# Performance work log

Measured on AMD Instinct MI355X. Metric: run time of the kernel, lower is better.

The kernel has to match this reference:

```python
import jax, jax.numpy as jnp
import numpy as np

D_MODEL = 1024
NHEAD = 16
HEAD_DIM = D_MODEL // NHEAD
DFF = 4096
EPS = 1e-5


def _layer_norm(x, gamma, beta):
    mu = jnp.mean(x, axis=-1, keepdims=True)
    var = jnp.mean(jnp.square(x - mu), axis=-1, keepdims=True)
    return (x - mu) * jax.lax.rsqrt(var + EPS) * gamma + beta


def setup_inputs() -> dict:
    key = jax.random.key(0)
    ks = jax.random.split(key, 16)
    s = 1.0 / np.sqrt(D_MODEL)
    sf = 1.0 / np.sqrt(DFF)
    inp = {
        "x": jax.random.normal(ks[0], (4, 4096, D_MODEL), dtype=jnp.float32),
        "wq": jax.random.uniform(ks[1], (D_MODEL, D_MODEL), jnp.float32, -s, s),
        "bq": jnp.zeros((D_MODEL,), jnp.float32),
        "wk": jax.random.uniform(ks[2], (D_MODEL, D_MODEL), jnp.float32, -s, s),
        "bk": jnp.zeros((D_MODEL,), jnp.float32),
        "wv": jax.random.uniform(ks[3], (D_MODEL, D_MODEL), jnp.float32, -s, s),
        "bv": jnp.zeros((D_MODEL,), jnp.float32),
        "wo": jax.random.uniform(ks[4], (D_MODEL, D_MODEL), jnp.float32, -s, s),
        "bo": jnp.zeros((D_MODEL,), jnp.float32),
        "w1": jax.random.uniform(ks[5], (D_MODEL, 2 * DFF), jnp.float32, -s, s),
        "b1": jnp.zeros((2 * DFF,), jnp.float32),
        "w2": jax.random.uniform(ks[6], (DFF, D_MODEL), jnp.float32, -sf, sf),
        "b2": jnp.zeros((D_MODEL,), jnp.float32),
        "g1": jnp.ones((D_MODEL,), jnp.float32),
        "be1": jnp.zeros((D_MODEL,), jnp.float32),
        "g2": jnp.ones((D_MODEL,), jnp.float32),
        "be2": jnp.zeros((D_MODEL,), jnp.float32),
    }
    return inp


def reference(x, wq, bq, wk, bk, wv, bv, wo, bo, w1, b1, w2, b2, g1, be1, g2, be2):
    B, S, _ = x.shape
    # --- sublayer 1: pre-norm + linear attention ---
    h = _layer_norm(x, g1, be1)
    q = (h @ wq + bq).reshape(B, S, NHEAD, HEAD_DIM).transpose(0, 2, 1, 3)
    k = (h @ wk + bk).reshape(B, S, NHEAD, HEAD_DIM).transpose(0, 2, 1, 3)
    v = (h @ wv + bv).reshape(B, S, NHEAD, HEAD_DIM).transpose(0, 2, 1, 3)
    q = jax.nn.elu(q) + 1.0
    k = jax.nn.elu(k) + 1.0
    # kv: [B,H,d,e] = sum_s k[...,s,d] v[...,s,e]  (O(n) linear attention)
    kv = jnp.einsum("bhsd,bhse->bhde", k, v)
    attn = jnp.einsum("bhsd,bhde->bhse", q, kv)
    attn = attn.transpose(0, 2, 1, 3).reshape(B, S, D_MODEL)
    x = x + (attn @ wo + bo)
    # --- sublayer 2: pre-norm + GEGLU FFN ---
    h = _layer_norm(x, g2, be2)
    ff = h @ w1 + b1
    g, lin = ff[..., :DFF], ff[..., DFF:]
    ff = jax.nn.gelu(g, approximate=False) * lin
    x = x + (ff @ w2 + b2)
    return x
```

## Files before the change

kernel.cpp:

```cpp
#include <hip/hip_runtime.h>

typedef unsigned short u16;
typedef u16  u16x2  __attribute__((ext_vector_type(2)));
typedef u16  u16x4  __attribute__((ext_vector_type(4)));
typedef u16  u16x8  __attribute__((ext_vector_type(8)));
typedef float f32x4 __attribute__((ext_vector_type(4)));
typedef __bf16 bf16x8 __attribute__((ext_vector_type(8)));

#define D_MODEL 1024
#define DFF     4096
#define SEQ     4096
#define BATCH   4
#define NHEAD   16
#define MROWS   (BATCH*SEQ)
#define MCHUNK  4096

#define BM 128
#define BN 128
#define BK 32

__device__ __forceinline__ float bf2f(u16 u) {
  unsigned v = ((unsigned)u) << 16;
  return __builtin_bit_cast(float, v);
}
__device__ __forceinline__ u16 f2bf(float f) {
  unsigned u = __builtin_bit_cast(unsigned, f);
  u += 0x7fffu + ((u >> 16) & 1u);
  return (u16)(u >> 16);
}

__device__ __forceinline__ void gload16(void* lds, const void* g) {
  __builtin_amdgcn_global_load_lds(
      (const __attribute__((address_space(1))) unsigned*)g,
      (__attribute__((address_space(3))) unsigned*)lds, 16, 0, 0);
}

__device__ __forceinline__ void barrier_raw() {
  asm volatile("" ::: "memory");
  __builtin_amdgcn_s_barrier();
  asm volatile("" ::: "memory");
}
#define VMWAIT(n) asm volatile("s_waitcnt vmcnt(" #n ")" ::: "memory")

__device__ __forceinline__ int xcd_swz_bid() {
  const int gx = gridDim.x;
  const int nwg = gx * gridDim.y;
  int bid = blockIdx.y * gx + blockIdx.x;
  const int cpx = nwg >> 3;
  return (bid & 7) * cpx + (bid >> 3);
}

__global__ __launch_bounds__(256)
void transpose_kernel(const float* __restrict__ W, u16* __restrict__ Wt, int K, int N)
{
  __shared__ u16 tile[32][33];
  const int n0 = blockIdx.x * 32, k0 = blockIdx.y * 32;
  const int tx = threadIdx.x & 31, ty = threadIdx.x >> 5;
#pragma unroll
  for (int r = ty; r < 32; r += 8)
    tile[r][tx] = f2bf(W[(size_t)(k0 + r) * N + n0 + tx]);
  __syncthreads();
#pragma unroll
  for (int r = ty; r < 32; r += 8)
    Wt[(size_t)(n0 + r) * K + k0 + tx] = tile[tx][r];
}

template<typename T>
__global__ __launch_bounds__(256)
void ln_kernel(const T* __restrict__ x, const float* __restrict__ g,
               const float* __restrict__ be, u16* __restrict__ out)
{
  const int row = blockIdx.x;
  const int t = threadIdx.x;
  float v0, v1, v2, v3;
  if constexpr (sizeof(T) == 4) {
    f32x4 u = ((const f32x4*)((const float*)x + (size_t)row * D_MODEL))[t];
    v0 = u.x; v1 = u.y; v2 = u.z; v3 = u.w;
  } else {
    u16x4 u = ((const u16x4*)((const u16*)x + (size_t)row * D_MODEL))[t];
    v0 = bf2f(u.x); v1 = bf2f(u.y); v2 = bf2f(u.z); v3 = bf2f(u.w);
  }
  float s  = v0 + v1 + v2 + v3;
  float s2 = v0*v0 + v1*v1 + v2*v2 + v3*v3;
#pragma unroll
  for (int off = 32; off > 0; off >>= 1) {
    s  += __shfl_down(s,  off);
    s2 += __shfl_down(s2, off);
  }
  __shared__ float red[8];
  if ((t & 63) == 0) { red[t >> 6] = s; red[4 + (t >> 6)] = s2; }
  __syncthreads();
  float S  = red[0] + red[1] + red[2] + red[3];
  float S2 = red[4] + red[5] + red[6] + red[7];
  float mu  = S * (1.f / D_MODEL);
  float var = S2 * (1.f / D_MODEL) - mu * mu;
  var = fmaxf(var, 0.f);
  float rs  = rsqrtf(var + 1e-5f);
  f32x4 gu = ((const f32x4*)g)[t];
  f32x4 bu = ((const f32x4*)be)[t];
  u16x4 o;
  o.x = f2bf((v0 - mu) * rs * gu.x + bu.x);
  o.y = f2bf((v1 - mu) * rs * gu.y + bu.y);
  o.z = f2bf((v2 - mu) * rs * gu.z + bu.z);
  o.w = f2bf((v3 - mu) * rs * gu.w + bu.w);
  ((u16x4*)(out + (size_t)row * D_MODEL))[t] = o;
}

template<int MODE>
__global__ __launch_bounds__(256, 2)
void gemm_kernel(const u16* __restrict__ A, const u16* __restrict__ Bt,
                 const float* __restrict__ bias, const void* __restrict__ resv,
                 void* __restrict__ outv, int N, int K)
{
  __shared__ __align__(16) u16 lA[3][BM * BK];
  __shared__ __align__(16) u16 lB[3][BN * BK];
  const float* resf = (const float*)resv;
  const u16*   resb = (const u16*)resv;
  const int tid = threadIdx.x;
  const int wave = tid >> 6, lane = tid & 63;
  const int quad = lane >> 4, ln = lane & 15;
  const int bid = xcd_swz_bid();
  const int bm = (bid / (int)gridDim.x) * BM, bn = (bid % (int)gridDim.x) * BN;
  const int wm = (wave >> 1) * 64, wn = (wave & 1) * 64;

  f32x4 acc[4][4] = {};

  const int c0 = tid,       r0 = c0 >> 2, q0 = c0 & 3;
  const int c1 = tid + 256, r1 = c1 >> 2, q1 = c1 & 3;
  const u16* gA0 = A  + (size_t)(bm + r0) * K + q0 * 8;
  const u16* gA1 = A  + (size_t)(bm + r1) * K + q1 * 8;
  const u16* gB0 = Bt + (size_t)(bn + r0) * K + q0 * 8;
  const u16* gB1 = Bt + (size_t)(bn + r1) * K + q1 * 8;
  const int d0 = wave * 64 * 8;
  const int d1 = (256 + wave * 64) * 8;

  const int nk = K / BK;
  gload16(&lA[0][d0], gA0);
  gload16(&lA[0][d1], gA1);
  gload16(&lB[0][d0], gB0);
  gload16(&lB[0][d1], gB1);
  gload16(&lA[1][d0], gA0 + BK);
  gload16(&lA[1][d1], gA1 + BK);
  gload16(&lB[1][d0], gB0 + BK);
  gload16(&lB[1][d1], gB1 + BK);

  int cur = 0;
  for (int t = 0; t < nk; ++t) {
    if (t + 2 < nk) {
      int wb = cur + 2; if (wb >= 3) wb -= 3;
      const size_t ko = (size_t)(t + 2) * BK;
      gload16(&lA[wb][d0], gA0 + ko);
      gload16(&lA[wb][d1], gA1 + ko);
      gload16(&lB[wb][d0], gB0 + ko);
      gload16(&lB[wb][d1], gB1 + ko);
      VMWAIT(8);
    } else if (t + 1 < nk) {
      VMWAIT(4);
    } else {
      VMWAIT(0);
    }
    barrier_raw();
    bf16x8 af[4], bfr[4];
#pragma unroll
    for (int i = 0; i < 4; ++i) {
      af[i]  = *(const bf16x8*)&lA[cur][(wm + i * 16 + ln) * BK + quad * 8];
      bfr[i] = *(const bf16x8*)&lB[cur][(wn + i * 16 + ln) * BK + quad * 8];
    }
#pragma unroll
    for (int i = 0; i < 4; ++i)
#pragma unroll
      for (int j = 0; j < 4; ++j)
        acc[i][j] = __builtin_amdgcn_mfma_f32_16x16x32_bf16(af[i], bfr[j], acc[i][j], 0, 0, 0);
    barrier_raw();
    cur = cur + 1; if (cur >= 3) cur = 0;
  }

#pragma unroll
  for (int j = 0; j < 4; ++j) {
    const int col = bn + wn + j * 16 + ln;
    const float bv = bias[col];
#pragma unroll
    for (int i = 0; i < 4; ++i) {
#pragma unroll
      for (int r = 0; r < 4; ++r) {
        const int row = bm + wm + i * 16 + quad * 4 + r;
        const size_t off = (size_t)row * N + col;
        float vv = acc[i][j][r] + bv;
        if (MODE == 1) vv = vv > 0.f ? vv + 1.f : __expf(vv);
        if (MODE == 2) vv += resf[off];
        if (MODE == 3) vv += bf2f(resb[off]);
        if (MODE == 3) ((float*)outv)[off] = vv;
        else           ((u16*)outv)[off]   = f2bf(vv);
      }
    }
  }
}

__global__ __launch_bounds__(256, 2)
void ffn1_kernel(const u16* __restrict__ A, const u16* __restrict__ Wt,
                 const float* __restrict__ b1, u16* __restrict__ out, int K)
{
  __shared__ __align__(16) u16 lA [2][BM * BK];
  __shared__ __align__(16) u16 lBg[2][BN * BK];
  __shared__ __align__(16) u16 lBl[2][BN * BK];
  const int tid = threadIdx.x;
  const int wave = tid >> 6, lane = tid & 63;
  const int quad = lane >> 4, ln = lane & 15;
  const int bm = blockIdx.y * BM, bn = blockIdx.x * BN;
  const int wm = (wave >> 1) * 64, wn = (wave & 1) * 64;

  f32x4 accg[4][4] = {};
  f32x4 accl[4][4] = {};

  const int c0 = tid,       r0 = c0 >> 2, q0 = c0 & 3;
  const int c1 = tid + 256, r1 = c1 >> 2, q1 = c1 & 3;
  const u16* gA0 = A  + (size_t)(bm + r0) * K + q0 * 8;
  const u16* gA1 = A  + (size_t)(bm + r1) * K + q1 * 8;
  const u16* gG0 = Wt + (size_t)(bn + r0) * K + q0 * 8;
  const u16* gG1 = Wt + (size_t)(bn + r1) * K + q1 * 8;
  const u16* gL0 = Wt + (size_t)(DFF + bn + r0) * K + q0 * 8;
  const u16* gL1 = Wt + (size_t)(DFF + bn + r1) * K + q1 * 8;
  const int d0 = wave * 64 * 8;
  const int d1 = (256 + wave * 64) * 8;

  const int nk = K / BK;
  gload16(&lA [0][d0], gA0);
  gload16(&lA [0][d1], gA1);
  gload16(&lBg[0][d0], gG0);
  gload16(&lBg[0][d1], gG1);
  gload16(&lBl[0][d0], gL0);
  gload16(&lBl[0][d1], gL1);

  int cur = 0;
  for (int t = 0; t < nk; ++t) {
    if (t + 1 < nk) {
      const int nxt = cur ^ 1;
      const size_t ko = (size_t)(t + 1) * BK;
      gload16(&lA [nxt][d0], gA0 + ko);
      gload16(&lA [nxt][d1], gA1 + ko);
      gload16(&lBg[nxt][d0], gG0 + ko);
      gload16(&lBg[nxt][d1], gG1 + ko);
      gload16(&lBl[nxt][d0], gL0 + ko);
      gload16(&lBl[nxt][d1], gL1 + ko);
      VMWAIT(6);
    } else {
      VMWAIT(0);
    }
    barrier_raw();
    bf16x8 af[4], bg[4], bl[4];
#pragma unroll
    for (int i = 0; i < 4; ++i) {
      af[i] = *(const bf16x8*)&lA [cur][(wm + i * 16 + ln) * BK + quad * 8];
      bg[i] = *(const bf16x8*)&lBg[cur][(wn + i * 16 + ln) * BK + quad * 8];
      bl[i] = *(const bf16x8*)&lBl[cur][(wn + i * 16 + ln) * BK + quad * 8];
    }
#pragma unroll
    for (int i = 0; i < 4; ++i)
#pragma unroll
      for (int j = 0; j < 4; ++j) {
        accg[i][j] = __builtin_amdgcn_mfma_f32_16x16x32_bf16(af[i], bg[j], accg[i][j], 0, 0, 0);
        accl[i][j] = __builtin_amdgcn_mfma_f32_16x16x32_bf16(af[i], bl[j], accl[i][j], 0, 0, 0);
      }
    barrier_raw();
    cur ^= 1;
  }

#pragma unroll
  for (int j = 0; j < 4; ++j) {
    const int col = bn + wn + j * 16 + ln;
    const float bgv = b1[col];
    const float blv = b1[DFF + col];
#pragma unroll
    for (int i = 0; i < 4; ++i) {
#pragma unroll
      for (int r = 0; r < 4; ++r) {
        const int row = bm + wm + i * 16 + quad * 4 + r;
        float gg = accg[i][j][r] + bgv;
        float ll = accl[i][j][r] + blv;
        float ge = 0.5f * gg * (1.f + erff(gg * 0.70710678118f));
        out[(size_t)row * DFF + col] = f2bf(ge * ll);
      }
    }
  }
}

#define KVCH 1024
__global__ __launch_bounds__(256)
void kvmm_kernel(const u16* __restrict__ kk, const u16* __restrict__ vv,
                 float* __restrict__ kvpart)
{
  __shared__ __align__(16) u16 lK[32][66];
  __shared__ __align__(16) u16 lV[32][66];
  const int blk = blockIdx.x;
  const int c = blk & 3, bh = blk >> 2;
  const int b = bh >> 4, h = bh & 15;
  const int tid = threadIdx.x, wave = tid >> 6, lane = tid & 63;
  const int quad = lane >> 4, ln = lane & 15;
  const int dbase = (wave >> 1) * 32, ebase = (wave & 1) * 32;
  f32x4 acc[2][2] = {};

  const int srow = tid >> 3;
  const int dcol = (tid & 7) * 8;
  const size_t gbase = ((size_t)b * SEQ + (size_t)c * KVCH + srow) * D_MODEL + h * 64 + dcol;
  const u16* gk = kk + gbase;
  const u16* gv = vv + gbase;

  for (int s0 = 0; s0 < KVCH; s0 += 32) {
    u16x8 k8 = *(const u16x8*)(gk + (size_t)s0 * D_MODEL);
    u16x8 v8 = *(const u16x8*)(gv + (size_t)s0 * D_MODEL);
    __syncthreads();
    u16x2* wk2 = (u16x2*)&lK[srow][dcol];
    u16x2* wv2 = (u16x2*)&lV[srow][dcol];
#pragma unroll
    for (int p = 0; p < 4; ++p) {
      u16x2 a; a.x = k8[2*p]; a.y = k8[2*p+1]; wk2[p] = a;
      u16x2 w; w.x = v8[2*p]; w.y = v8[2*p+1]; wv2[p] = w;
    }
    __syncthreads();
    bf16x8 af[2], bf[2];
#pragma unroll
    for (int i = 0; i < 2; ++i) {
      const int dd = dbase + i * 16 + ln;
      const int ee = ebase + i * 16 + ln;
      u16x8 at, bt;
#pragma unroll
      for (int j = 0; j < 8; ++j) {
        at[j] = lK[quad * 8 + j][dd];
        bt[j] = lV[quad * 8 + j][ee];
      }
      af[i] = __builtin_bit_cast(bf16x8, at);
      bf[i] = __builtin_bit_cast(bf16x8, bt);
    }
#pragma unroll
    for (int i = 0; i < 2; ++i)
#pragma unroll
      for (int j = 0; j < 2; ++j)
        acc[i][j] = __builtin_amdgcn_mfma_f32_16x16x32_bf16(af[i], bf[j], acc[i][j], 0, 0, 0);
  }

  float* op = kvpart + ((size_t)c * 64 + bh) * 4096;
#pragma unroll
  for (int i = 0; i < 2; ++i)
#pragma unroll
    for (int j = 0; j < 2; ++j)
#pragma unroll
      for (int r = 0; r < 4; ++r) {
        const int d = dbase + i * 16 + quad * 4 + r;
        const int e = ebase + j * 16 + ln;
        op[d * 64 + e] = acc[i][j][r];
      }
}

__global__ __launch_bounds__(256)
void kvreduce_kernel(float* __restrict__ p)
{
  const int i = blockIdx.x * 256 + threadIdx.x;
  f32x4* p4 = (f32x4*)p;
  f32x4 a = p4[i];
  f32x4 b = p4[i + 65536];
  f32x4 c = p4[i + 131072];
  f32x4 d = p4[i + 196608];
  p4[i] = (a + b) + (c + d);
}

__global__ __launch_bounds__(256)
void attn_kernel(const u16* __restrict__ qq, const float* __restrict__ kv,
                 u16* __restrict__ out)
{
  __shared__ __align__(16) float kvs[64 * 64];
  const int blk = blockIdx.x;
  const int sc = blk & 63;
  const int bh = blk >> 6;
  const int b = bh >> 4, h = bh & 15;
  const int t = threadIdx.x;
  const f32x4* src = (const f32x4*)(kv + (size_t)bh * 4096);
  for (int i = t; i < 1024; i += 256) ((f32x4*)kvs)[i] = src[i];
  __syncthreads();
  const int sl = t >> 2, e0 = (t & 3) * 16;
  const size_t row = (size_t)b * SEQ + sc * 64 + sl;
  const u16* qp = qq + row * D_MODEL + h * 64;
  float qv[64];
#pragma unroll
  for (int i = 0; i < 16; ++i) {
    u16x4 u = ((const u16x4*)qp)[i];
    qv[i*4+0] = bf2f(u.x); qv[i*4+1] = bf2f(u.y);
    qv[i*4+2] = bf2f(u.z); qv[i*4+3] = bf2f(u.w);
  }
  f32x4 acc[4] = {};
  for (int d = 0; d < 64; ++d) {
    const float qd = qv[d];
    const f32x4* kr = (const f32x4*)(kvs + d * 64 + e0);
#pragma unroll
    for (int i = 0; i < 4; ++i) acc[i] += qd * kr[i];
  }
  u16* op = out + row * D_MODEL + h * 64 + e0;
#pragma unroll
  for (int i = 0; i < 4; ++i) {
    u16x4 o;
    o.x = f2bf(acc[i][0]); o.y = f2bf(acc[i][1]);
    o.z = f2bf(acc[i][2]); o.w = f2bf(acc[i][3]);
    ((u16x4*)op)[i] = o;
  }
}

extern "C" void kernel_launch(void* const* d_in, const int* in_sizes, int n_in,
                              void* d_out, int out_size, void* d_ws, size_t ws_size,
                              hipStream_t stream)
{
  const float* x   = (const float*)d_in[0];
  const float* wq  = (const float*)d_in[1];
  const float* bq  = (const float*)d_in[2];
  const float* wk  = (const float*)d_in[3];
  const float* bk  = (const float*)d_in[4];
  const float* wv  = (const float*)d_in[5];
  const float* bv  = (const float*)d_in[6];
  const float* wo  = (const float*)d_in[7];
  const float* bo  = (const float*)d_in[8];
  const float* w1  = (const float*)d_in[9];
  const float* b1  = (const float*)d_in[10];
  const float* w2  = (const float*)d_in[11];
  const float* b2  = (const float*)d_in[12];
  const float* g1  = (const float*)d_in[13];
  const float* be1 = (const float*)d_in[14];
  const float* g2  = (const float*)d_in[15];
  const float* be2 = (const float*)d_in[16];

  char* ws = (char*)d_ws;
  const size_t MB = 1024ull * 1024ull;
  u16* wqt = (u16*)(ws + 0 * MB);
  u16* wkt = (u16*)(ws + 2 * MB);
  u16* wvt = (u16*)(ws + 4 * MB);
  u16* wot = (u16*)(ws + 6 * MB);
  u16* w1t = (u16*)(ws + 8 * MB);
  u16* w2t = (u16*)(ws + 24 * MB);

  u16* hb    = (u16*)(ws + 32 * MB);
  u16* x1b   = (u16*)(ws + 32 * MB);
  u16* kb    = (u16*)(ws + 64 * MB);
  u16* qb    = (u16*)(ws + 64 * MB);
  u16* hb2   = (u16*)(ws + 64 * MB);
  u16* vb    = (u16*)(ws + 96 * MB);
  u16* attnb = (u16*)(ws + 96 * MB);
  u16* gbuf  = (u16*)(ws + 96 * MB);
  float* kvpart = (float*)(ws + 2 * MB);

  transpose_kernel<<<dim3(32, 32), 256, 0, stream>>>(wq, wqt, 1024, 1024);
  transpose_kernel<<<dim3(32, 32), 256, 0, stream>>>(wk, wkt, 1024, 1024);
  transpose_kernel<<<dim3(32, 32), 256, 0, stream>>>(wv, wvt, 1024, 1024);
  transpose_kernel<<<dim3(32, 32), 256, 0, stream>>>(wo, wot, 1024, 1024);
  transpose_kernel<<<dim3(256, 32), 256, 0, stream>>>(w1, w1t, 1024, 8192);
  transpose_kernel<<<dim3(32, 128), 256, 0, stream>>>(w2, w2t, 4096, 1024);

  ln_kernel<float><<<MROWS, 256, 0, stream>>>(x, g1, be1, hb);

  dim3 gproj(D_MODEL / BN, MROWS / BM);
  gemm_kernel<1><<<gproj, 256, 0, stream>>>(hb, wkt, bk, nullptr, kb, D_MODEL, D_MODEL);
  gemm_kernel<0><<<gproj, 256, 0, stream>>>(hb, wvt, bv, nullptr, vb, D_MODEL, D_MODEL);

  kvmm_kernel<<<64 * 4, 256, 0, stream>>>(kb, vb, kvpart);
  kvreduce_kernel<<<256, 256, 0, stream>>>(kvpart);

  gemm_kernel<1><<<gproj, 256, 0, stream>>>(hb, wqt, bq, nullptr, qb, D_MODEL, D_MODEL);

  attn_kernel<<<BATCH * NHEAD * (SEQ / 64), 256, 0, stream>>>(qb, kvpart, attnb);

  gemm_kernel<2><<<gproj, 256, 0, stream>>>(attnb, wot, bo, x, x1b, D_MODEL, D_MODEL);

  ln_kernel<u16><<<MROWS, 256, 0, stream>>>(x1b, g2, be2, hb2);

  for (int c = 0; c < MROWS / MCHUNK; ++c) {
    const size_t ro = (size_t)c * MCHUNK;
    ffn1_kernel<<<dim3(DFF / BN, MCHUNK / BM), 256, 0, stream>>>(
        hb2 + ro * D_MODEL, w1t, b1, gbuf, D_MODEL);
    gemm_kernel<3><<<dim3(D_MODEL / BN, MCHUNK / BM), 256, 0, stream>>>(
        gbuf, w2t, b2, x1b + ro * D_MODEL, (float*)d_out + ro * D_MODEL, D_MODEL, DFF);
  }
}
```

Before: 1.115 ms.

## Template GEMM on N-tile width and process two K-tiles per barrier pair

Result: faster. 1.015 ms (-9.0%).

```diff
diff --git a/kernel.cpp b/kernel.cpp
--- a/kernel.cpp
+++ b/kernel.cpp
@@ -16,7 +16,6 @@
 #define MCHUNK  4096
 
 #define BM 128
-#define BN 128
 #define BK 32
 
 __device__ __forceinline__ float bf2f(u16 u) {
@@ -106,24 +105,25 @@
   ((u16x4*)(out + (size_t)row * D_MODEL))[t] = o;
 }
 
-template<int MODE>
+template<int MODE, int BNT>
 __global__ __launch_bounds__(256, 2)
 void gemm_kernel(const u16* __restrict__ A, const u16* __restrict__ Bt,
                  const float* __restrict__ bias, const void* __restrict__ resv,
                  void* __restrict__ outv, int N, int K)
 {
-  __shared__ __align__(16) u16 lA[3][BM * BK];
-  __shared__ __align__(16) u16 lB[3][BN * BK];
+  constexpr int NJ = BNT / 32;
+  __shared__ __align__(16) u16 lA[4][BM * BK];
+  __shared__ __align__(16) u16 lB[4][BNT * BK];
   const float* resf = (const float*)resv;
   const u16*   resb = (const u16*)resv;
   const int tid = threadIdx.x;
   const int wave = tid >> 6, lane = tid & 63;
   const int quad = lane >> 4, ln = lane & 15;
   const int bid = xcd_swz_bid();
-  const int bm = (bid / (int)gridDim.x) * BM, bn = (bid % (int)gridDim.x) * BN;
-  const int wm = (wave >> 1) * 64, wn = (wave & 1) * 64;
-
-  f32x4 acc[4][4] = {};
+  const int bm = (bid / (int)gridDim.x) * BM, bn = (bid % (int)gridDim.x) * BNT;
+  const int wm = (wave >> 1) * 64, wn = (wave & 1) * (BNT / 2);
+
+  f32x4 acc[4][NJ] = {};
 
   const int c0 = tid,       r0 = c0 >> 2, q0 = c0 & 3;
   const int c1 = tid + 256, r1 = c1 >> 2, q1 = c1 & 3;
@@ -134,49 +134,49 @@
   const int d0 = wave * 64 * 8;
   const int d1 = (256 + wave * 64) * 8;
 
-  const int nk = K / BK;
-  gload16(&lA[0][d0], gA0);
-  gload16(&lA[0][d1], gA1);
-  gload16(&lB[0][d0], gB0);
-  gload16(&lB[0][d1], gB1);
-  gload16(&lA[1][d0], gA0 + BK);
-  gload16(&lA[1][d1], gA1 + BK);
-  gload16(&lB[1][d0], gB0 + BK);
-  gload16(&lB[1][d1], gB1 + BK);
-
-  int cur = 0;
-  for (int t = 0; t < nk; ++t) {
-    if (t + 2 < nk) {
-      int wb = cur + 2; if (wb >= 3) wb -= 3;
-      const size_t ko = (size_t)(t + 2) * BK;
-      gload16(&lA[wb][d0], gA0 + ko);
-      gload16(&lA[wb][d1], gA1 + ko);
-      gload16(&lB[wb][d0], gB0 + ko);
-      gload16(&lB[wb][d1], gB1 + ko);
-      VMWAIT(8);
-    } else if (t + 1 < nk) {
-      VMWAIT(4);
+  auto stage = [&](int b, size_t ko) {
+    gload16(&lA[b][d0], gA0 + ko);
+    gload16(&lA[b][d1], gA1 + ko);
+    gload16(&lB[b][d0], gB0 + ko);
+    if constexpr (BNT == 128) gload16(&lB[b][d1], gB1 + ko);
+  };
+  auto compute = [&](int b) {
+    bf16x8 af[4], bfr[NJ];
+#pragma unroll
+    for (int i = 0; i < 4; ++i)
+      af[i] = *(const bf16x8*)&lA[b][(wm + i * 16 + ln) * BK + quad * 8];
+#pragma unroll
+    for (int j = 0; j < NJ; ++j)
+      bfr[j] = *(const bf16x8*)&lB[b][(wn + j * 16 + ln) * BK + quad * 8];
+#pragma unroll
+    for (int i = 0; i < 4; ++i)
+#pragma unroll
+      for (int j = 0; j < NJ; ++j)
+        acc[i][j] = __builtin_amdgcn_mfma_f32_16x16x32_bf16(af[i], bfr[j], acc[i][j], 0, 0, 0);
+  };
+
+  const int ni = K / 64;
+  stage(0, 0);
+  stage(1, BK);
+
+  for (int i = 0; i < ni; ++i) {
+    const int b0 = (i & 1) * 2, b1 = b0 + 1;
+    if (i + 1 < ni) {
+      const size_t ko = (size_t)(i + 1) * 64;
+      stage(b0 ^ 2, ko);
+      stage(b1 ^ 2, ko + BK);
+      if constexpr (BNT == 128) { VMWAIT(8); } else { VMWAIT(6); }
     } else {
       VMWAIT(0);
     }
     barrier_raw();
-    bf16x8 af[4], bfr[4];
-#pragma unroll
-    for (int i = 0; i < 4; ++i) {
-      af[i]  = *(const bf16x8*)&lA[cur][(wm + i * 16 + ln) * BK + quad * 8];
-      bfr[i] = *(const bf16x8*)&lB[cur][(wn + i * 16 + ln) * BK + quad * 8];
-    }
-#pragma unroll
-    for (int i = 0; i < 4; ++i)
-#pragma unroll
-      for (int j = 0; j < 4; ++j)
-        acc[i][j] = __builtin_amdgcn_mfma_f32_16x16x32_bf16(af[i], bfr[j], acc[i][j], 0, 0, 0);
+    compute(b0);
+    compute(b1);
     barrier_raw();
-    cur = cur + 1; if (cur >= 3) cur = 0;
-  }
-
-#pragma unroll
-  for (int j = 0; j < 4; ++j) {
+  }
+
+#pragma unroll
+  for (int j = 0; j < NJ; ++j) {
     const int col = bn + wn + j * 16 + ln;
     const float bv = bias[col];
 #pragma unroll
@@ -201,12 +201,12 @@
                  const float* __restrict__ b1, u16* __restrict__ out, int K)
 {
   __shared__ __align__(16) u16 lA [2][BM * BK];
-  __shared__ __align__(16) u16 lBg[2][BN * BK];
-  __shared__ __align__(16) u16 lBl[2][BN * BK];
+  __shared__ __align__(16) u16 lBg[2][BM * BK];
+  __shared__ __align__(16) u16 lBl[2][BM * BK];
   const int tid = threadIdx.x;
   const int wave = tid >> 6, lane = tid & 63;
   const int quad = lane >> 4, ln = lane & 15;
-  const int bm = blockIdx.y * BM, bn = blockIdx.x * BN;
+  const int bm = blockIdx.y * BM, bn = blockIdx.x * BM;
   const int wm = (wave >> 1) * 64, wn = (wave & 1) * 64;
 
   f32x4 accg[4][4] = {};
@@ -453,26 +453,26 @@
 
   ln_kernel<float><<<MROWS, 256, 0, stream>>>(x, g1, be1, hb);
 
-  dim3 gproj(D_MODEL / BN, MROWS / BM);
-  gemm_kernel<1><<<gproj, 256, 0, stream>>>(hb, wkt, bk, nullptr, kb, D_MODEL, D_MODEL);
-  gemm_kernel<0><<<gproj, 256, 0, stream>>>(hb, wvt, bv, nullptr, vb, D_MODEL, D_MODEL);
+  dim3 gproj(D_MODEL / 128, MROWS / BM);
+  gemm_kernel<1,128><<<gproj, 256, 0, stream>>>(hb, wkt, bk, nullptr, kb, D_MODEL, D_MODEL);
+  gemm_kernel<0,128><<<gproj, 256, 0, stream>>>(hb, wvt, bv, nullptr, vb, D_MODEL, D_MODEL);
 
   kvmm_kernel<<<64 * 4, 256, 0, stream>>>(kb, vb, kvpart);
   kvreduce_kernel<<<256, 256, 0, stream>>>(kvpart);
 
-  gemm_kernel<1><<<gproj, 256, 0, stream>>>(hb, wqt, bq, nullptr, qb, D_MODEL, D_MODEL);
+  gemm_kernel<1,128><<<gproj, 256, 0, stream>>>(hb, wqt, bq, nullptr, qb, D_MODEL, D_MODEL);
 
   attn_kernel<<<BATCH * NHEAD * (SEQ / 64), 256, 0, stream>>>(qb, kvpart, attnb);
 
-  gemm_kernel<2><<<gproj, 256, 0, stream>>>(attnb, wot, bo, x, x1b, D_MODEL, D_MODEL);
+  gemm_kernel<2,128><<<gproj, 256, 0, stream>>>(attnb, wot, bo, x, x1b, D_MODEL, D_MODEL);
 
   ln_kernel<u16><<<MROWS, 256, 0, stream>>>(x1b, g2, be2, hb2);
 
   for (int c = 0; c < MROWS / MCHUNK; ++c) {
     const size_t ro = (size_t)c * MCHUNK;
-    ffn1_kernel<<<dim3(DFF / BN, MCHUNK / BM), 256, 0, stream>>>(
+    ffn1_kernel<<<dim3(DFF / 128, MCHUNK / BM), 256, 0, stream>>>(
         hb2 + ro * D_MODEL, w1t, b1, gbuf, D_MODEL);
-    gemm_kernel<3><<<dim3(D_MODEL / BN, MCHUNK / BM), 256, 0, stream>>>(
+    gemm_kernel<3,64><<<dim3(D_MODEL / 64, MCHUNK / BM), 256, 0, stream>>>(
         gbuf, w2t, b2, x1b + ro * D_MODEL, (float*)d_out + ro * D_MODEL, D_MODEL, DFF);
   }
 }
```
